# Kernel optimization log

Hardware: AMD Instinct MI355X
Metric: run time of the kernel (lower is better)

Reference implementation:

```python
import jax, jax.numpy as jnp
import numpy as np

# Tree: 64 leaves (16 feat -> 16 out), 8 mids (16 feat + 8*16 child = 144 -> 32 out),
# root (16 feat + 8*32 child = 272 -> 64 out), head -> 10 tasks. Eval-mode BatchNorm.
B = 16384
EPS = 1e-5


def setup_inputs() -> dict:
    key = jax.random.key(0)
    ks = jax.random.split(key, 24)
    rn = lambda k, s: jax.random.normal(k, s, dtype=jnp.float32)
    ru = lambda k, s: jax.random.uniform(k, s, dtype=jnp.float32)
    return {
        "x": rn(ks[0], (B, 1168)),
        # leaf layers (64 nodes, 16 -> 16)
        "Wl": rn(ks[1], (64, 16, 16)) * 0.1, "bl": rn(ks[2], (64, 16)) * 0.1,
        "gl": ru(ks[3], (64, 16)) + 0.5, "betal": rn(ks[4], (64, 16)) * 0.1,
        "ml": rn(ks[5], (64, 16)) * 0.1, "vl": ru(ks[6], (64, 16)) + 0.5,
        # mid layers (8 nodes, 144 -> 32)
        "Wm": rn(ks[7], (8, 144, 32)) * 0.1, "bm": rn(ks[8], (8, 32)) * 0.1,
        "gm": ru(ks[9], (8, 32)) + 0.5, "betam": rn(ks[10], (8, 32)) * 0.1,
        "mm": rn(ks[11], (8, 32)) * 0.1, "vm": ru(ks[12], (8, 32)) + 0.5,
        # root layer (272 -> 64)
        "Wr": rn(ks[13], (272, 64)) * 0.1, "br": rn(ks[14], (64,)) * 0.1,
        "gr": ru(ks[15], (64,)) + 0.5, "betar": rn(ks[16], (64,)) * 0.1,
        "mr": rn(ks[17], (64,)) * 0.1, "vr": ru(ks[18], (64,)) + 0.5,
        # root prediction head (64 -> 10 tasks)
        "Wh": rn(ks[19], (64, 10)) * 0.1, "bh": rn(ks[20], (10,)) * 0.1,
    }


def _bn(h, g, b, m, v):
    return (h - m) * jax.lax.rsqrt(v + EPS) * g + b


def reference(x, Wl, bl, gl, betal, ml, vl, Wm, bm, gm, betam, mm, vm,
              Wr, br, gr, betar, mr, vr, Wh, bh):
    n = x.shape[0]
    # leaves: gather own features (contiguous layout), Linear+BN+Tanh, batched over 64 nodes
    xl = x[:, :1024].reshape(n, 64, 16)
    hl = jnp.tanh(_bn(jnp.einsum('bli,lio->blo', xl, Wl) + bl, gl, betal, ml, vl))
    # mids: concat own features with 8 leaf-child outputs -> [n, 8, 144]
    xm = x[:, 1024:1152].reshape(n, 8, 16)
    mid_in = jnp.concatenate([xm, hl.reshape(n, 8, 128)], axis=-1)
    hm = jnp.tanh(_bn(jnp.einsum('bmi,mio->bmo', mid_in, Wm) + bm, gm, betam, mm, vm))
    # root: concat own features with 8 mid outputs -> [n, 272]
    root_in = jnp.concatenate([x[:, 1152:1168], hm.reshape(n, 256)], axis=-1)
    hr = jnp.tanh(_bn(root_in @ Wr + br, gr, betar, mr, vr))
    # root prediction head (eval-mode forward returns only root prediction)
    return hr @ Wh + bh
```

## Files before the change

### kernel.cpp

```cpp
#include <hip/hip_runtime.h>
#include <hip/hip_bf16.h>

typedef __attribute__((ext_vector_type(8))) short bf16x8;
typedef __attribute__((ext_vector_type(4))) float f32x4;

#define EPS 1e-5f
#define K2L 2.8853900817779268f

#define N_FRAG_BLOCKS 182
#define WSB_LEAF 0
#define WSB_MID  64
#define WSB_ROOT 144
#define WSB_HEAD 180
#define ST_SL 0
#define ST_TL 1024
#define ST_SM 2048
#define ST_TM 2304
#define ST_SR 2560
#define ST_TR 2624
#define WS_ST_BYTE_OFF (N_FRAG_BLOCKS * 1024)

#define XSW 1192

__device__ __forceinline__ unsigned short f2bf(float f) {
    unsigned u = __float_as_uint(f);
    unsigned r = u + 0x7fffu + ((u >> 16) & 1u);
    return (unsigned short)(r >> 16);
}

__device__ __forceinline__ unsigned pk2(float a, float b) {
    float2 f2; f2.x = a; f2.y = b;
    __hip_bfloat162 h = __float22bfloat162_rn(f2);
    union { __hip_bfloat162 h2; unsigned u; } cv; cv.h2 = h;
    return cv.u;
}

__device__ __forceinline__ float bn_act(float acc, float Sp, float Tp) {
    float e = exp2f(fmaf(acc, Sp, Tp));
    float r = __builtin_amdgcn_rcpf(e + 1.0f);
    return fmaf(-2.0f, r, 1.0f);
}

__global__ void ontology_prep(
    const float* __restrict__ Wl, const float* __restrict__ Wm,
    const float* __restrict__ Wr, const float* __restrict__ Wh,
    const float* __restrict__ bl, const float* __restrict__ gl,
    const float* __restrict__ betal, const float* __restrict__ ml,
    const float* __restrict__ vl,
    const float* __restrict__ bm, const float* __restrict__ gm,
    const float* __restrict__ betam, const float* __restrict__ mm,
    const float* __restrict__ vm,
    const float* __restrict__ br, const float* __restrict__ gr,
    const float* __restrict__ betar, const float* __restrict__ mr,
    const float* __restrict__ vr,
    unsigned short* __restrict__ wsFrag, float* __restrict__ wsST)
{
    const int tid = threadIdx.x;
    if (blockIdx.x < 46) {
        const int b = blockIdx.x * 4 + (tid >> 6);
        if (b >= N_FRAG_BLOCKS) return;
        const int t = tid & 63;
        const int row = t & 15, g = t >> 4;
        unsigned short vals[8];
        #pragma unroll
        for (int i = 0; i < 8; ++i) {
            const int k = g * 8 + i;
            float v = 0.f;
            if (b < 64) {
                const int l = b;
                if ((l & 1) == 0) { if (k < 16)  v = Wl[l * 256 + k * 16 + row]; }
                else              { if (k >= 16) v = Wl[l * 256 + (k - 16) * 16 + row]; }
            } else if (b < 144) {
                const int idx = b - 64, m = idx / 10, rem = idx % 10;
                const int tt = rem / 5, s = rem % 5;
                const int j = s * 32 + k;
                const int krow = (j < 128) ? (16 + j) : ((j < 144) ? (j - 128) : -1);
                if (krow >= 0) v = Wm[m * 4608 + krow * 32 + tt * 16 + row];
            } else if (b < 180) {
                const int idx = b - 144, tt = idx / 9, s = idx % 9;
                if (s == 0) { if (k < 16) v = Wr[k * 64 + tt * 16 + row]; }
                else { const int krow = 16 + (s - 1) * 32 + k;
                       v = Wr[krow * 64 + tt * 16 + row]; }
            } else {
                const int s = b - 180, krow = s * 32 + k;
                if (row < 10) v = Wh[krow * 10 + row];
            }
            vals[i] = f2bf(v);
        }
        #pragma unroll
        for (int i = 0; i < 8; ++i) wsFrag[b * 512 + t * 8 + i] = vals[i];
    } else {
        #pragma unroll
        for (int i = 0; i < 4; ++i) {
            const int id = tid + 256 * i;
            const float S = gl[id] * rsqrtf(vl[id] + EPS);
            wsST[ST_SL + id] = S * K2L;
            wsST[ST_TL + id] = ((bl[id] - ml[id]) * S + betal[id]) * K2L;
        }
        {
            const int id = tid;
            const float S = gm[id] * rsqrtf(vm[id] + EPS);
            wsST[ST_SM + id] = S * K2L;
            wsST[ST_TM + id] = ((bm[id] - mm[id]) * S + betam[id]) * K2L;
        }
        if (tid < 64) {
            const int id = tid;
            const float S = gr[id] * rsqrtf(vr[id] + EPS);
            wsST[ST_SR + id] = S * K2L;
            wsST[ST_TR + id] = ((br[id] - mr[id]) * S + betar[id]) * K2L;
        }
    }
}

__global__ __launch_bounds__(512, 8) void ontology_mfma(
    const float* __restrict__ x,
    const unsigned short* __restrict__ wsFrag,
    const float* __restrict__ wsST,
    const float* __restrict__ bh,
    float* __restrict__ out)
{
    __shared__ __align__(16) unsigned short xs[16 * XSW];

    const int tid  = threadIdx.x;
    const int w    = tid >> 6;
    const int lane = tid & 63;
    const int c    = lane & 15;
    const int g    = lane >> 4;
    const int rowbase = blockIdx.x * 16;

    const float* Sl = wsST + ST_SL; const float* Tl = wsST + ST_TL;
    const float* Sm = wsST + ST_SM; const float* Tm = wsST + ST_TM;
    const float* Sr = wsST + ST_SR; const float* Tr = wsST + ST_TR;

    {
        const int srow = tid >> 5;
        const int j    = tid & 31;
        const float4* xr4 = (const float4*)(x + (size_t)(rowbase + srow) * 1168);
        unsigned short* xsrow = xs + srow * XSW;

        float4 v0, v1, v2, v3, v4;
        v0 = xr4[j];       v1 = xr4[j + 32];  v2 = xr4[j + 64];
        v3 = xr4[j + 96];  v4 = xr4[j + 128];
        {
            uint2 p;
            p.x = pk2(v0.x, v0.y); p.y = pk2(v0.z, v0.w); *(uint2*)(xsrow + (j      ) * 4) = p;
            p.x = pk2(v1.x, v1.y); p.y = pk2(v1.z, v1.w); *(uint2*)(xsrow + (j +  32) * 4) = p;
            p.x = pk2(v2.x, v2.y); p.y = pk2(v2.z, v2.w); *(uint2*)(xsrow + (j +  64) * 4) = p;
            p.x = pk2(v3.x, v3.y); p.y = pk2(v3.z, v3.w); *(uint2*)(xsrow + (j +  96) * 4) = p;
            p.x = pk2(v4.x, v4.y); p.y = pk2(v4.z, v4.w); *(uint2*)(xsrow + (j + 128) * 4) = p;
        }
        v0 = xr4[j + 160]; v1 = xr4[j + 192]; v2 = xr4[j + 224]; v3 = xr4[j + 256];
        const bool has9 = (j < 4);
        if (has9) v4 = xr4[j + 288];
        {
            uint2 p;
            p.x = pk2(v0.x, v0.y); p.y = pk2(v0.z, v0.w); *(uint2*)(xsrow + (j + 160) * 4) = p;
            p.x = pk2(v1.x, v1.y); p.y = pk2(v1.z, v1.w); *(uint2*)(xsrow + (j + 192) * 4) = p;
            p.x = pk2(v2.x, v2.y); p.y = pk2(v2.z, v2.w); *(uint2*)(xsrow + (j + 224) * 4) = p;
            p.x = pk2(v3.x, v3.y); p.y = pk2(v3.z, v3.w); *(uint2*)(xsrow + (j + 256) * 4) = p;
            if (has9) {
                p.x = pk2(v4.x, v4.y); p.y = pk2(v4.z, v4.w);
                *(uint2*)(xsrow + (j + 288) * 4) = p;
            }
        }
        if (tid < 64) {
            const int zr = tid >> 2, seg = tid & 3;
            uint2 z; z.x = 0u; z.y = 0u;
            *(uint2*)(xs + zr * XSW + 1168 + seg * 4) = z;
        }
    }
    __syncthreads();

    const int colbase = w * 128;
    #pragma unroll
    for (int p = 0; p < 4; ++p) {
        bf16x8 bfrag = *(const bf16x8*)(xs + c * XSW + colbase + p * 32 + g * 8);
        #pragma unroll
        for (int e = 0; e < 2; ++e) {
            const int l = 2 * p + e, leaf = w * 8 + l;
            bf16x8 afrag = *(const bf16x8*)(wsFrag + (WSB_LEAF + leaf) * 512 + lane * 8);
            f32x4 zz = {0.f,0.f,0.f,0.f};
            f32x4 acc = __builtin_amdgcn_mfma_f32_16x16x32_bf16(afrag, bfrag, zz, 0, 0, 0);
            const int po = leaf * 16 + 4 * g;
            float4 S = *(const float4*)(Sl + po);
            float4 T = *(const float4*)(Tl + po);
            uint2 pk;
            pk.x = pk2(bn_act(acc[0], S.x, T.x), bn_act(acc[1], S.y, T.y));
            pk.y = pk2(bn_act(acc[2], S.z, T.z), bn_act(acc[3], S.w, T.w));
            *(uint2*)(xs + c * XSW + colbase + l * 16 + 4 * g) = pk;
        }
    }

    {
        f32x4 acc0 = {0.f,0.f,0.f,0.f};
        f32x4 acc1 = {0.f,0.f,0.f,0.f};
        const unsigned short* fb = wsFrag + (WSB_MID + w * 10) * 512 + lane * 8;
        #pragma unroll
        for (int s = 0; s < 5; ++s) {
            const int cc = (s < 4) ? (colbase + s * 32) : (1024 + w * 16);
            bf16x8 bfrag = *(const bf16x8*)(xs + c * XSW + cc + g * 8);
            bf16x8 a0 = *(const bf16x8*)(fb + s * 512);
            bf16x8 a1 = *(const bf16x8*)(fb + (5 + s) * 512);
            acc0 = __builtin_amdgcn_mfma_f32_16x16x32_bf16(a0, bfrag, acc0, 0, 0, 0);
            acc1 = __builtin_amdgcn_mfma_f32_16x16x32_bf16(a1, bfrag, acc1, 0, 0, 0);
        }
        #pragma unroll
        for (int tt = 0; tt < 2; ++tt) {
            f32x4 acc = tt ? acc1 : acc0;
            const int po = w * 32 + tt * 16 + 4 * g;
            float4 S = *(const float4*)(Sm + po);
            float4 T = *(const float4*)(Tm + po);
            uint2 pk;
            pk.x = pk2(bn_act(acc[0], S.x, T.x), bn_act(acc[1], S.y, T.y));
            pk.y = pk2(bn_act(acc[2], S.z, T.z), bn_act(acc[3], S.w, T.w));
            *(uint2*)(xs + c * XSW + colbase + tt * 16 + 4 * g) = pk;
        }
    }
    __syncthreads();

    if (w < 4) {
        const unsigned short* fb = wsFrag + (WSB_ROOT + w * 9) * 512 + lane * 8;
        f32x4 acc = {0.f,0.f,0.f,0.f};
        {
            bf16x8 bfrag = *(const bf16x8*)(xs + c * XSW + 1152 + g * 8);
            bf16x8 a0 = *(const bf16x8*)fb;
            acc = __builtin_amdgcn_mfma_f32_16x16x32_bf16(a0, bfrag, acc, 0, 0, 0);
        }
        #pragma unroll
        for (int s = 1; s <= 8; ++s) {
            bf16x8 bfrag = *(const bf16x8*)(xs + c * XSW + (s - 1) * 128 + g * 8);
            bf16x8 a0 = *(const bf16x8*)(fb + s * 512);
            acc = __builtin_amdgcn_mfma_f32_16x16x32_bf16(a0, bfrag, acc, 0, 0, 0);
        }
        const int po = w * 16 + 4 * g;
        float4 S = *(const float4*)(Sr + po);
        float4 T = *(const float4*)(Tr + po);
        uint2 pk;
        pk.x = pk2(bn_act(acc[0], S.x, T.x), bn_act(acc[1], S.y, T.y));
        pk.y = pk2(bn_act(acc[2], S.z, T.z), bn_act(acc[3], S.w, T.w));
        *(uint2*)(xs + c * XSW + 32 + w * 16 + 4 * g) = pk;
    }
    __syncthreads();

    if (w == 0) {
        f32x4 acc = {0.f,0.f,0.f,0.f};
        #pragma unroll
        for (int s = 0; s < 2; ++s) {
            bf16x8 bfrag = *(const bf16x8*)(xs + c * XSW + 32 + s * 32 + g * 8);
            bf16x8 a0 = *(const bf16x8*)(wsFrag + (WSB_HEAD + s) * 512 + lane * 8);
            acc = __builtin_amdgcn_mfma_f32_16x16x32_bf16(a0, bfrag, acc, 0, 0, 0);
        }
        float* op = out + (size_t)(rowbase + c) * 10 + 4 * g;
        if (g < 2) {
            float2 o1 = {acc[0] + bh[4 * g],     acc[1] + bh[4 * g + 1]};
            float2 o2 = {acc[2] + bh[4 * g + 2], acc[3] + bh[4 * g + 3]};
            *(float2*)op = o1;
            *(float2*)(op + 2) = o2;
        } else if (g == 2) {
            float2 o1 = {acc[0] + bh[8], acc[1] + bh[9]};
            *(float2*)op = o1;
        }
    }
}

extern "C" void kernel_launch(void* const* d_in, const int* in_sizes, int n_in,
                              void* d_out, int out_size, void* d_ws, size_t ws_size,
                              hipStream_t stream) {
    const float* x     = (const float*)d_in[0];
    const float* Wl    = (const float*)d_in[1];
    const float* bl    = (const float*)d_in[2];
    const float* gl    = (const float*)d_in[3];
    const float* betal = (const float*)d_in[4];
    const float* ml    = (const float*)d_in[5];
    const float* vl    = (const float*)d_in[6];
    const float* Wm    = (const float*)d_in[7];
    const float* bm    = (const float*)d_in[8];
    const float* gm    = (const float*)d_in[9];
    const float* betam = (const float*)d_in[10];
    const float* mm    = (const float*)d_in[11];
    const float* vm    = (const float*)d_in[12];
    const float* Wr    = (const float*)d_in[13];
    const float* br    = (const float*)d_in[14];
    const float* gr    = (const float*)d_in[15];
    const float* betar = (const float*)d_in[16];
    const float* mr    = (const float*)d_in[17];
    const float* vr    = (const float*)d_in[18];
    const float* Wh    = (const float*)d_in[19];
    const float* bh    = (const float*)d_in[20];
    float* out = (float*)d_out;

    unsigned short* wsFrag = (unsigned short*)d_ws;
    float* wsST = (float*)((char*)d_ws + WS_ST_BYTE_OFF);

    ontology_prep<<<47, 256, 0, stream>>>(
        Wl, Wm, Wr, Wh, bl, gl, betal, ml, vl, bm, gm, betam, mm, vm,
        br, gr, betar, mr, vr, wsFrag, wsST);

    const int n = in_sizes[0] / 1168;
    ontology_mfma<<<n / 16, 512, 0, stream>>>(x, wsFrag, wsST, bh, out);
}
```

Baseline: 31.69 us.

## Fuse weight-prep kernel into main kernel with global atomic flag handoff

Removes the separate prep launch: the first 24 blocks of the main kernel repack weights and BN scale/shift into the workspace, then bump a global counter. Every block stages its x tile first and then spins on that counter before using the prepared data, so prep overlaps the x load. A memset of the flag replaces the prep launch. This relies on the prep blocks being scheduled and making progress, since otherwise the spinning blocks could deadlock, and it adds atomic polling traffic.

```diff
diff --git a/kernel.cpp b/kernel.cpp
--- a/kernel.cpp
+++ b/kernel.cpp
@@ -19,6 +19,8 @@
 #define ST_SR 2560
 #define ST_TR 2624
 #define WS_ST_BYTE_OFF (N_FRAG_BLOCKS * 1024)
+#define FLAG_BYTE_OFF  197632
+#define NPREP 24
 
 #define XSW 1192
 
@@ -41,7 +43,8 @@
     return fmaf(-2.0f, r, 1.0f);
 }
 
-__global__ void ontology_prep(
+__global__ __launch_bounds__(512, 8) void ontology_fused(
+    const float* __restrict__ x,
     const float* __restrict__ Wl, const float* __restrict__ Wm,
     const float* __restrict__ Wr, const float* __restrict__ Wh,
     const float* __restrict__ bl, const float* __restrict__ gl,
@@ -53,84 +56,83 @@
     const float* __restrict__ br, const float* __restrict__ gr,
     const float* __restrict__ betar, const float* __restrict__ mr,
     const float* __restrict__ vr,
-    unsigned short* __restrict__ wsFrag, float* __restrict__ wsST)
-{
-    const int tid = threadIdx.x;
-    if (blockIdx.x < 46) {
-        const int b = blockIdx.x * 4 + (tid >> 6);
-        if (b >= N_FRAG_BLOCKS) return;
-        const int t = tid & 63;
-        const int row = t & 15, g = t >> 4;
-        unsigned short vals[8];
-        #pragma unroll
-        for (int i = 0; i < 8; ++i) {
-            const int k = g * 8 + i;
-            float v = 0.f;
-            if (b < 64) {
-                const int l = b;
-                if ((l & 1) == 0) { if (k < 16)  v = Wl[l * 256 + k * 16 + row]; }
-                else              { if (k >= 16) v = Wl[l * 256 + (k - 16) * 16 + row]; }
-            } else if (b < 144) {
-                const int idx = b - 64, m = idx / 10, rem = idx % 10;
-                const int tt = rem / 5, s = rem % 5;
-                const int j = s * 32 + k;
-                const int krow = (j < 128) ? (16 + j) : ((j < 144) ? (j - 128) : -1);
-                if (krow >= 0) v = Wm[m * 4608 + krow * 32 + tt * 16 + row];
-            } else if (b < 180) {
-                const int idx = b - 144, tt = idx / 9, s = idx % 9;
-                if (s == 0) { if (k < 16) v = Wr[k * 64 + tt * 16 + row]; }
-                else { const int krow = 16 + (s - 1) * 32 + k;
-                       v = Wr[krow * 64 + tt * 16 + row]; }
-            } else {
-                const int s = b - 180, krow = s * 32 + k;
-                if (row < 10) v = Wh[krow * 10 + row];
-            }
-            vals[i] = f2bf(v);
-        }
-        #pragma unroll
-        for (int i = 0; i < 8; ++i) wsFrag[b * 512 + t * 8 + i] = vals[i];
-    } else {
-        #pragma unroll
-        for (int i = 0; i < 4; ++i) {
-            const int id = tid + 256 * i;
-            const float S = gl[id] * rsqrtf(vl[id] + EPS);
-            wsST[ST_SL + id] = S * K2L;
-            wsST[ST_TL + id] = ((bl[id] - ml[id]) * S + betal[id]) * K2L;
-        }
-        {
-            const int id = tid;
-            const float S = gm[id] * rsqrtf(vm[id] + EPS);
-            wsST[ST_SM + id] = S * K2L;
-            wsST[ST_TM + id] = ((bm[id] - mm[id]) * S + betam[id]) * K2L;
-        }
-        if (tid < 64) {
-            const int id = tid;
-            const float S = gr[id] * rsqrtf(vr[id] + EPS);
-            wsST[ST_SR + id] = S * K2L;
-            wsST[ST_TR + id] = ((br[id] - mr[id]) * S + betar[id]) * K2L;
-        }
-    }
-}
-
-__global__ __launch_bounds__(512, 8) void ontology_mfma(
-    const float* __restrict__ x,
-    const unsigned short* __restrict__ wsFrag,
-    const float* __restrict__ wsST,
     const float* __restrict__ bh,
+    unsigned short* __restrict__ wsFrag, float* __restrict__ wsST,
+    int* __restrict__ flagp,
     float* __restrict__ out)
 {
     __shared__ __align__(16) unsigned short xs[16 * XSW];
 
     const int tid  = threadIdx.x;
+    const int bid  = blockIdx.x;
     const int w    = tid >> 6;
     const int lane = tid & 63;
     const int c    = lane & 15;
     const int g    = lane >> 4;
-    const int rowbase = blockIdx.x * 16;
-
-    const float* Sl = wsST + ST_SL; const float* Tl = wsST + ST_TL;
-    const float* Sm = wsST + ST_SM; const float* Tm = wsST + ST_TM;
-    const float* Sr = wsST + ST_SR; const float* Tr = wsST + ST_TR;
+    const int rowbase = bid * 16;
+
+    if (bid < NPREP) {
+        if (bid < 23) {
+            const int b = bid * 8 + (tid >> 6);
+            if (b < N_FRAG_BLOCKS) {
+                const int t = tid & 63;
+                const int row = t & 15, gg = t >> 4;
+                unsigned short vals[8];
+                #pragma unroll
+                for (int i = 0; i < 8; ++i) {
+                    const int k = gg * 8 + i;
+                    float v = 0.f;
+                    if (b < 64) {
+                        const int l = b;
+                        if ((l & 1) == 0) { if (k < 16)  v = Wl[l * 256 + k * 16 + row]; }
+                        else              { if (k >= 16) v = Wl[l * 256 + (k - 16) * 16 + row]; }
+                    } else if (b < 144) {
+                        const int idx = b - 64, m = idx / 10, rem = idx % 10;
+                        const int tt = rem / 5, s = rem % 5;
+                        const int j = s * 32 + k;
+                        const int krow = (j < 128) ? (16 + j) : ((j < 144) ? (j - 128) : -1);
+                        if (krow >= 0) v = Wm[m * 4608 + krow * 32 + tt * 16 + row];
+                    } else if (b < 180) {
+                        const int idx = b - 144, tt = idx / 9, s = idx % 9;
+                        if (s == 0) { if (k < 16) v = Wr[k * 64 + tt * 16 + row]; }
+                        else { const int krow = 16 + (s - 1) * 32 + k;
+                               v = Wr[krow * 64 + tt * 16 + row]; }
+                    } else {
+                        const int s = b - 180, krow = s * 32 + k;
+                        if (row < 10) v = Wh[krow * 10 + row];
+                    }
+                    vals[i] = f2bf(v);
+                }
+                #pragma unroll
+                for (int i = 0; i < 8; ++i) wsFrag[b * 512 + t * 8 + i] = vals[i];
+            }
+        } else if (tid < 256) {
+            #pragma unroll
+            for (int i = 0; i < 4; ++i) {
+                const int id = tid + 256 * i;
+                const float S = gl[id] * rsqrtf(vl[id] + EPS);
+                wsST[ST_SL + id] = S * K2L;
+                wsST[ST_TL + id] = ((bl[id] - ml[id]) * S + betal[id]) * K2L;
+            }
+            {
+                const int id = tid;
+                const float S = gm[id] * rsqrtf(vm[id] + EPS);
+                wsST[ST_SM + id] = S * K2L;
+                wsST[ST_TM + id] = ((bm[id] - mm[id]) * S + betam[id]) * K2L;
+            }
+            if (tid < 64) {
+                const int id = tid;
+                const float S = gr[id] * rsqrtf(vr[id] + EPS);
+                wsST[ST_SR + id] = S * K2L;
+                wsST[ST_TR + id] = ((br[id] - mr[id]) * S + betar[id]) * K2L;
+            }
+        }
+        __syncthreads();
+        if (tid == 0) {
+            __threadfence();
+            atomicAdd(flagp, 1);
+        }
+    }
 
     {
         const int srow = tid >> 5;
@@ -169,7 +171,16 @@
             *(uint2*)(xs + zr * XSW + 1168 + seg * 4) = z;
         }
     }
+
+    if (tid == 0) {
+        while (__hip_atomic_load(flagp, __ATOMIC_ACQUIRE, __HIP_MEMORY_SCOPE_AGENT) < NPREP)
+            __builtin_amdgcn_s_sleep(2);
+    }
     __syncthreads();
+
+    const float* Sl = wsST + ST_SL; const float* Tl = wsST + ST_TL;
+    const float* Sm = wsST + ST_SM; const float* Tm = wsST + ST_TM;
+    const float* Sr = wsST + ST_SR; const float* Tr = wsST + ST_TR;
 
     const int colbase = w * 128;
     #pragma unroll
@@ -291,11 +302,12 @@
 
     unsigned short* wsFrag = (unsigned short*)d_ws;
     float* wsST = (float*)((char*)d_ws + WS_ST_BYTE_OFF);
-
-    ontology_prep<<<47, 256, 0, stream>>>(
-        Wl, Wm, Wr, Wh, bl, gl, betal, ml, vl, bm, gm, betam, mm, vm,
-        br, gr, betar, mr, vr, wsFrag, wsST);
+    int* flagp = (int*)((char*)d_ws + FLAG_BYTE_OFF);
+
+    hipMemsetAsync(flagp, 0, 4, stream);
 
     const int n = in_sizes[0] / 1168;
-    ontology_mfma<<<n / 16, 512, 0, stream>>>(x, wsFrag, wsST, bh, out);
-}
+    ontology_fused<<<n / 16, 512, 0, stream>>>(
+        x, Wl, Wm, Wr, Wh, bl, gl, betal, ml, vl, bm, gm, betam, mm, vm,
+        br, gr, betar, mr, vr, bh, wsFrag, wsST, flagp, out);
+}
```

Result: slower. 68.10 us (+114.9%).
